# Optimization experiments

Measured on AMD Instinct MI355X. Metric: run time of the kernel, lower is better.

## Reference

```python
import jax, jax.numpy as jnp
import numpy as np

P = 8192          # number of gaussians
H = 256           # image height
W = 256           # image width
TANX = 0.5        # tan(fovx/2)
TANY = 0.5        # tan(fovy/2)
SCALE_MOD = 1.0
CHUNK = 128       # gaussians composited per scan step
FX = W / (2.0 * TANX)   # focal_x, as in forward()
FY = H / (2.0 * TANY)   # focal_y


def setup_inputs() -> dict:
    key = jax.random.key(0)
    k = jax.random.split(key, 6)
    # place gaussians in the camera frustum (camera at origin, looking +z)
    z = jax.random.uniform(k[0], (P,), minval=2.0, maxval=6.0)
    xy = jax.random.normal(k[1], (P, 2)) * 0.4 * (z * TANX)[:, None]
    means3D = jnp.concatenate([xy, z[:, None]], axis=1)
    scales = 0.01 + 0.04 * jax.random.uniform(k[2], (P, 3))
    rotations = jax.random.normal(k[3], (P, 4))  # normalized inside reference
    opacities = 0.05 + 0.9 * jax.random.uniform(k[4], (P, 1))
    colors_precomp = jax.random.uniform(k[5], (P, 3))
    background = jnp.zeros((3,), jnp.float32)
    viewmatrix = jnp.eye(4, dtype=jnp.float32)  # row-vector convention: p' = [p,1] @ V
    znear, zfar = 0.01, 100.0
    Pm = np.zeros((4, 4), np.float32)
    Pm[0, 0] = 1.0 / TANX
    Pm[1, 1] = 1.0 / TANY
    Pm[2, 2] = zfar / (zfar - znear)
    Pm[2, 3] = -(zfar * znear) / (zfar - znear)
    Pm[3, 2] = 1.0
    projmatrix = jnp.asarray(Pm.T)  # row-vector convention (full proj = proj @ view, view = I)
    return dict(means3D=means3D, colors_precomp=colors_precomp, opacities=opacities,
                scales=scales, rotations=rotations, background=background,
                viewmatrix=viewmatrix, projmatrix=projmatrix)


def _quat_to_rot(q):
    q = q / jnp.linalg.norm(q, axis=-1, keepdims=True)
    r, x, y, z = q[:, 0], q[:, 1], q[:, 2], q[:, 3]
    R = jnp.stack([
        1 - 2 * (y * y + z * z), 2 * (x * y - r * z), 2 * (x * z + r * y),
        2 * (x * y + r * z), 1 - 2 * (x * x + z * z), 2 * (y * z - r * x),
        2 * (x * z - r * y), 2 * (y * z + r * x), 1 - 2 * (x * x + y * y)], axis=-1)
    return R.reshape(-1, 3, 3)


def _forward(means3D, colors_precomp, opacities, scales, rotations, background,
             viewmatrix, projmatrix):
    Pn = means3D.shape[0]
    # --- preprocess: 3D covariance from scale/rotation ---
    R = _quat_to_rot(rotations)
    s2 = (scales * SCALE_MOD) ** 2
    Sigma = jnp.einsum('pij,pj,pkj->pik', R, s2, R)  # R diag(s^2) R^T, [P,3,3]
    hom = jnp.concatenate([means3D, jnp.ones((Pn, 1), means3D.dtype)], axis=1)
    p_view = (hom @ viewmatrix)[:, :3]
    p_hom = hom @ projmatrix
    p_proj = p_hom[:, :3] / (p_hom[:, 3:4] + 1e-7)
    # NDC -> pixel centers
    mean2d = jnp.stack([((p_proj[:, 0] + 1.0) * W - 1.0) * 0.5,
                        ((p_proj[:, 1] + 1.0) * H - 1.0) * 0.5], axis=1)
    depths = p_view[:, 2]
    # --- EWA splatting: project covariance to 2D ---
    Rv = viewmatrix[:3, :3]
    cov_cam = jnp.einsum('ji,pjk,kl->pil', Rv, Sigma, Rv)  # Rv^T Sigma Rv
    tz = p_view[:, 2]
    tx = jnp.clip(p_view[:, 0] / tz, -1.3 * TANX, 1.3 * TANX) * tz
    ty = jnp.clip(p_view[:, 1] / tz, -1.3 * TANY, 1.3 * TANY) * tz
    zero = jnp.zeros_like(tz)
    J = jnp.stack([jnp.stack([FX / tz, zero, -FX * tx / tz ** 2], -1),
                   jnp.stack([zero, FY / tz, -FY * ty / tz ** 2], -1)], axis=1)  # [P,2,3]
    cov2d = jnp.einsum('pij,pjk,plk->pil', J, cov_cam, J)
    a = cov2d[:, 0, 0] + 0.3  # low-pass dilation as in 3DGS
    b = cov2d[:, 0, 1]
    c = cov2d[:, 1, 1] + 0.3
    det = a * c - b * b
    conic = jnp.stack([c, -b, a], axis=-1) / det[:, None]
    # --- global depth sort ---
    order = jnp.argsort(depths)
    m2d = mean2d[order]
    con = conic[order]
    col = colors_precomp[order]
    op = opacities[order]
    # --- per-pixel front-to-back alpha compositing ---
    px, py = jnp.meshgrid(jnp.arange(W, dtype=jnp.float32),
                          jnp.arange(H, dtype=jnp.float32))
    pixf = jnp.stack([px.ravel(), py.ravel()], axis=-1)  # [HW,2]
    n_chunks = Pn // CHUNK
    xs = (m2d.reshape(n_chunks, CHUNK, 2), con.reshape(n_chunks, CHUNK, 3),
          col.reshape(n_chunks, CHUNK, 3), op.reshape(n_chunks, CHUNK, 1))

    def step(carry, x):
        accum, T = carry
        m, cn, cl, o = x
        d = m[:, None, :] - pixf[None]  # [C,HW,2]
        power = (-0.5 * (cn[:, 0:1] * d[..., 0] ** 2 + cn[:, 2:3] * d[..., 1] ** 2)
                 - cn[:, 1:2] * d[..., 0] * d[..., 1])
        alpha = jnp.minimum(0.99, o * jnp.exp(power))
        alpha = jnp.where((power > 0.0) | (alpha < 1.0 / 255.0), 0.0, alpha)
        cp = jnp.cumprod(1.0 - alpha, axis=0)  # within-chunk transmittance
        excl = jnp.concatenate([jnp.ones((1, alpha.shape[1]), alpha.dtype), cp[:-1]], 0)
        wgt = alpha * excl * T[None]
        accum = accum + jnp.einsum('cp,cd->pd', wgt, cl)
        return (accum, T * cp[-1]), None

    accum0 = jnp.zeros((H * W, 3), jnp.float32)
    T0 = jnp.ones((H * W,), jnp.float32)
    (accum, T), _ = jax.lax.scan(step, (accum0, T0), xs)
    out = accum + T[:, None] * background[None]
    return out.reshape(H, W, 3).transpose(2, 0, 1)  # [3,H,W]


def reference(means3D, colors_precomp, opacities, scales, rotations, background,
              viewmatrix, projmatrix):
    return _forward(means3D, colors_precomp, opacities, scales, rotations,
                    background, viewmatrix, projmatrix)
```

## Files before the change

### kernel.cpp

```cpp
#include <hip/hip_runtime.h>


#define PN 8192
#define IH 256
#define IW 256


__global__ __launch_bounds__(256) void preprocess_kernel(
    const float* __restrict__ means, const float* __restrict__ colors,
    const float* __restrict__ ops, const float* __restrict__ scales,
    const float* __restrict__ rots, const float* __restrict__ V,
    const float* __restrict__ Pm, float* __restrict__ ws)
{
    int i = blockIdx.x * 256 + threadIdx.x;
    if (i >= PN) return;

    float mx3 = means[3 * i], my3 = means[3 * i + 1], mz3 = means[3 * i + 2];
    float qr = rots[4 * i], qx = rots[4 * i + 1], qy = rots[4 * i + 2], qz = rots[4 * i + 3];
    float qn = 1.0f / sqrtf(qr * qr + qx * qx + qy * qy + qz * qz);
    float r = qr * qn, x = qx * qn, y = qy * qn, z = qz * qn;

    float R00 = 1.f - 2.f * (y * y + z * z), R01 = 2.f * (x * y - r * z), R02 = 2.f * (x * z + r * y);
    float R10 = 2.f * (x * y + r * z), R11 = 1.f - 2.f * (x * x + z * z), R12 = 2.f * (y * z - r * x);
    float R20 = 2.f * (x * z - r * y), R21 = 2.f * (y * z + r * x), R22 = 1.f - 2.f * (x * x + y * y);

    float s0 = scales[3 * i];     s0 *= s0;
    float s1 = scales[3 * i + 1]; s1 *= s1;
    float s2 = scales[3 * i + 2]; s2 *= s2;

    float Sg[3][3];
    Sg[0][0] = R00 * R00 * s0 + R01 * R01 * s1 + R02 * R02 * s2;
    Sg[0][1] = R00 * R10 * s0 + R01 * R11 * s1 + R02 * R12 * s2;
    Sg[0][2] = R00 * R20 * s0 + R01 * R21 * s1 + R02 * R22 * s2;
    Sg[1][1] = R10 * R10 * s0 + R11 * R11 * s1 + R12 * R12 * s2;
    Sg[1][2] = R10 * R20 * s0 + R11 * R21 * s1 + R12 * R22 * s2;
    Sg[2][2] = R20 * R20 * s0 + R21 * R21 * s1 + R22 * R22 * s2;
    Sg[1][0] = Sg[0][1]; Sg[2][0] = Sg[0][2]; Sg[2][1] = Sg[1][2];

    float pv0 = mx3 * V[0] + my3 * V[4] + mz3 * V[8]  + V[12];
    float pv1 = mx3 * V[1] + my3 * V[5] + mz3 * V[9]  + V[13];
    float pv2 = mx3 * V[2] + my3 * V[6] + mz3 * V[10] + V[14];
    float ph0 = mx3 * Pm[0] + my3 * Pm[4] + mz3 * Pm[8]  + Pm[12];
    float ph1 = mx3 * Pm[1] + my3 * Pm[5] + mz3 * Pm[9]  + Pm[13];
    float ph3 = mx3 * Pm[3] + my3 * Pm[7] + mz3 * Pm[11] + Pm[15];
    float pw = 1.0f / (ph3 + 1e-7f);
    float m2x = ((ph0 * pw + 1.0f) * (float)IW - 1.0f) * 0.5f;
    float m2y = ((ph1 * pw + 1.0f) * (float)IH - 1.0f) * 0.5f;

    float Rv[3][3];
#pragma unroll
    for (int rr = 0; rr < 3; ++rr)
#pragma unroll
        for (int cc2 = 0; cc2 < 3; ++cc2) Rv[rr][cc2] = V[rr * 4 + cc2];
    float M[3][3];
#pragma unroll
    for (int j = 0; j < 3; ++j)
#pragma unroll
        for (int l = 0; l < 3; ++l)
            M[j][l] = Sg[j][0] * Rv[0][l] + Sg[j][1] * Rv[1][l] + Sg[j][2] * Rv[2][l];
    float cc[3][3];
#pragma unroll
    for (int ii = 0; ii < 3; ++ii)
#pragma unroll
        for (int l = 0; l < 3; ++l)
            cc[ii][l] = Rv[0][ii] * M[0][l] + Rv[1][ii] * M[1][l] + Rv[2][ii] * M[2][l];

    const float FX = 256.0f, FY = 256.0f;
    float tz = pv2;
    float itz = 1.0f / tz;
    float limx = 0.65f, limy = 0.65f;
    float txz = fminf(fmaxf(pv0 * itz, -limx), limx);
    float tyz = fminf(fmaxf(pv1 * itz, -limy), limy);
    float tx = txz * tz, ty = tyz * tz;
    float J00 = FX * itz, J02 = -FX * tx * itz * itz;
    float J11 = FY * itz, J12 = -FY * ty * itz * itz;

    float u00 = J00 * cc[0][0] + J02 * cc[2][0];
    float u01 = J00 * cc[0][1] + J02 * cc[2][1];
    float u02 = J00 * cc[0][2] + J02 * cc[2][2];
    float u11 = J11 * cc[1][1] + J12 * cc[2][1];
    float u12 = J11 * cc[1][2] + J12 * cc[2][2];
    float cov00 = u00 * J00 + u02 * J02;
    float cov01 = u01 * J11 + u02 * J12;
    float cov11 = u11 * J11 + u12 * J12;

    float a = cov00 + 0.3f;
    float b = cov01;
    float c = cov11 + 0.3f;
    float det = a * c - b * b;
    float idet = 1.0f / det;
    float cA = c * idet;
    float cB = -b * idet;
    float cC = a * idet;

    float ex = sqrtf(11.2f * a);
    float ey = sqrtf(11.2f * c);
    int x0 = max(0,  (int)floorf((m2x - ex) * 0.125f));
    int x1 = min(31, (int)floorf((m2x + ex) * 0.125f));
    int y0 = max(0,  (int)floorf((m2y - ey) * 0.125f));
    int y1 = min(31, (int)floorf((m2y + ey) * 0.125f));
    x0 = min(x0, 31); y0 = min(y0, 31); x1 = max(x1, 0); y1 = max(y1, 0);
    unsigned box = (unsigned)x0 | ((unsigned)x1 << 8) | ((unsigned)y0 << 16) | ((unsigned)y1 << 24);

    ws[i] = pv2;
    float4* preA = (float4*)(ws + PN);
    float4* preB = (float4*)(ws + 5 * PN);
    preA[i] = make_float4(m2x, m2y, cA, cB);
    preB[i] = make_float4(cC, ops[i], colors[3 * i], colors[3 * i + 1]);
    ws[9 * PN + i] = colors[3 * i + 2];
    ((unsigned*)(ws + 10 * PN))[i] = box;
}

__global__ __launch_bounds__(256) void sort_scatter_kernel(float* __restrict__ ws)
{
    const float* dep = ws;
    const float4* d4 = (const float4*)ws;
    int lane = threadIdx.x & 63;
    int wid = threadIdx.x >> 6;
    int gbase = blockIdx.x * 16 + wid * 4;

    float di0 = dep[gbase], di1 = dep[gbase + 1], di2 = dep[gbase + 2], di3 = dep[gbase + 3];
    int r0 = 0, r1 = 0, r2 = 0, r3 = 0;
#pragma unroll 4
    for (int k = 0; k < 32; ++k) {
        int j4 = k * 64 + lane;
        float4 d = d4[j4];
        int jb = j4 * 4;
        r0 += (d.x < di0) || (d.x == di0 && (jb    ) < gbase);
        r0 += (d.y < di0) || (d.y == di0 && (jb + 1) < gbase);
        r0 += (d.z < di0) || (d.z == di0 && (jb + 2) < gbase);
        r0 += (d.w < di0) || (d.w == di0 && (jb + 3) < gbase);
        r1 += (d.x < di1) || (d.x == di1 && (jb    ) < gbase + 1);
        r1 += (d.y < di1) || (d.y == di1 && (jb + 1) < gbase + 1);
        r1 += (d.z < di1) || (d.z == di1 && (jb + 2) < gbase + 1);
        r1 += (d.w < di1) || (d.w == di1 && (jb + 3) < gbase + 1);
        r2 += (d.x < di2) || (d.x == di2 && (jb    ) < gbase + 2);
        r2 += (d.y < di2) || (d.y == di2 && (jb + 1) < gbase + 2);
        r2 += (d.z < di2) || (d.z == di2 && (jb + 2) < gbase + 2);
        r2 += (d.w < di2) || (d.w == di2 && (jb + 3) < gbase + 2);
        r3 += (d.x < di3) || (d.x == di3 && (jb    ) < gbase + 3);
        r3 += (d.y < di3) || (d.y == di3 && (jb + 1) < gbase + 3);
        r3 += (d.z < di3) || (d.z == di3 && (jb + 2) < gbase + 3);
        r3 += (d.w < di3) || (d.w == di3 && (jb + 3) < gbase + 3);
    }
#pragma unroll
    for (int off = 1; off < 64; off <<= 1) {
        r0 += __shfl_xor(r0, off);
        r1 += __shfl_xor(r1, off);
        r2 += __shfl_xor(r2, off);
        r3 += __shfl_xor(r3, off);
    }
    if (lane < 4) {
        int rk = (lane == 0) ? r0 : (lane == 1) ? r1 : (lane == 2) ? r2 : r3;
        int i = gbase + lane;
        const float4* preA = (const float4*)(ws + PN);
        const float4* preB = (const float4*)(ws + 5 * PN);
        float4* sA = (float4*)(ws + 11 * PN);
        float4* sB = (float4*)(ws + 15 * PN);
        sA[rk] = preA[i];
        sB[rk] = preB[i];
        ws[19 * PN + rk] = ws[9 * PN + i];
        ((unsigned*)(ws + 20 * PN))[rk] = ((const unsigned*)(ws + 10 * PN))[i];
    }
}

__global__ __launch_bounds__(256) void raster_kernel(
    const float* __restrict__ ws, const float* __restrict__ bg,
    float* __restrict__ out)
{
    __shared__ float4 lsA[4][256];
    __shared__ float4 lsB[4][256];
    __shared__ float  lsb[4][256];
    volatile __shared__ float waveT[4];

    int tid = threadIdx.x;
    int lane = tid & 63, w = tid >> 6;
    int bq = blockIdx.x >> 8;
    int tileIdx = (bq << 8) | ((blockIdx.x & 255) ^ ((bq * 9) & 31));
    int tileX = tileIdx & 31, tileY = tileIdx >> 5;
    int px = tileX * 8 + (lane & 7), py = tileY * 8 + (lane >> 3);
    float pxf = (float)px, pyf = (float)py;

    const float4* sA = (const float4*)(ws + 11 * PN);
    const float4* sB = (const float4*)(ws + 15 * PN);
    const float* sb = ws + 19 * PN;
    const unsigned* sbox = (const unsigned*)(ws + 20 * PN);

    if (tid < 4) waveT[tid] = 1.0f;
    __syncthreads();

    float T = 1.0f, ar = 0.0f, ag = 0.0f, ab = 0.0f;

    for (int chunk = w * 8; chunk < w * 8 + 8; ++chunk) {
        float pre = 1.0f;
        for (int q = 0; q < w; ++q) pre *= waveT[q];
        if (pre < 1e-4f) break;

        int base = chunk * 256;
        unsigned long long wv[4];
#pragma unroll
        for (int k = 0; k < 4; ++k) {
            unsigned bx = sbox[base + k * 64 + lane];
            bool ov = (tileX >= (int)(bx & 255)) & (tileX <= (int)((bx >> 8) & 255)) &
                      (tileY >= (int)((bx >> 16) & 255)) & (tileY <= (int)(bx >> 24));
            wv[k] = __ballot(ov);
        }
        if (!(wv[0] | wv[1] | wv[2] | wv[3])) continue;

        int cnt = 0;
#pragma unroll
        for (int k = 0; k < 4; ++k) {
            unsigned long long wk = wv[k];
            if ((wk >> lane) & 1ull) {
                int slot = cnt + (int)__popcll(wk & ((1ull << lane) - 1ull));
                int g = base + k * 64 + lane;
                lsA[w][slot] = sA[g];
                lsB[w][slot] = sB[g];
                lsb[w][slot] = sb[g];
            }
            cnt += (int)__popcll(wk);
        }
        asm volatile("s_waitcnt lgkmcnt(0)" ::: "memory");

        int j = 0;
        for (; j + 1 < cnt; j += 2) {
            float4 A0 = lsA[w][j],     B0 = lsB[w][j];
            float4 A1 = lsA[w][j + 1], B1 = lsB[w][j + 1];
            float b0 = lsb[w][j], b1 = lsb[w][j + 1];
            float dx0 = A0.x - pxf, dy0 = A0.y - pyf;
            float dx1 = A1.x - pxf, dy1 = A1.y - pyf;
            float p0 = -0.5f * (A0.z * dx0 * dx0 + B0.x * dy0 * dy0) - A0.w * dx0 * dy0;
            float p1 = -0.5f * (A1.z * dx1 * dx1 + B1.x * dy1 * dy1) - A1.w * dx1 * dy1;
            float al0 = fminf(0.99f, B0.y * __expf(p0));
            float al1 = fminf(0.99f, B1.y * __expf(p1));
            float a0 = ((p0 > 0.0f) | (al0 < (1.0f / 255.0f))) ? 0.0f : al0;
            float a1 = ((p1 > 0.0f) | (al1 < (1.0f / 255.0f))) ? 0.0f : al1;
            float w0 = a0 * T;
            float Tm = T * (1.0f - a0);
            float w1 = a1 * Tm;
            ar = fmaf(w0, B0.z, ar); ar = fmaf(w1, B1.z, ar);
            ag = fmaf(w0, B0.w, ag); ag = fmaf(w1, B1.w, ag);
            ab = fmaf(w0, b0, ab);   ab = fmaf(w1, b1, ab);
            T = Tm * (1.0f - a1);
        }
        if (j < cnt) {
            float4 A = lsA[w][j];
            float4 B = lsB[w][j];
            float bcol = lsb[w][j];
            float dx = A.x - pxf, dy = A.y - pyf;
            float power = -0.5f * (A.z * dx * dx + B.x * dy * dy) - A.w * dx * dy;
            float alpha = fminf(0.99f, B.y * __expf(power));
            float a2 = ((power > 0.0f) | (alpha < (1.0f / 255.0f))) ? 0.0f : alpha;
            float wgt = a2 * T;
            ar = fmaf(wgt, B.z, ar);
            ag = fmaf(wgt, B.w, ag);
            ab = fmaf(wgt, bcol, ab);
            T *= (1.0f - a2);
        }
        asm volatile("s_waitcnt lgkmcnt(0)" ::: "memory");

        if (__all(T < 1e-5f)) break;

        float tmax = T;
#pragma unroll
        for (int off = 1; off < 64; off <<= 1) tmax = fmaxf(tmax, __shfl_xor(tmax, off));
        if (lane == 0) waveT[w] = tmax;
    }

    lsb[w][lane * 4 + 0] = ar;
    lsb[w][lane * 4 + 1] = ag;
    lsb[w][lane * 4 + 2] = ab;
    lsb[w][lane * 4 + 3] = T;
    __syncthreads();

    if (w == 0) {
        float A0 = 0.f, A1 = 0.f, A2 = 0.f, Tt = 1.f;
#pragma unroll
        for (int q = 0; q < 4; ++q) {
            A0 += Tt * lsb[q][lane * 4 + 0];
            A1 += Tt * lsb[q][lane * 4 + 1];
            A2 += Tt * lsb[q][lane * 4 + 2];
            Tt *= lsb[q][lane * 4 + 3];
        }
        int pidx = py * IW + px;
        out[pidx]               = A0 + Tt * bg[0];
        out[IH * IW + pidx]     = A1 + Tt * bg[1];
        out[2 * IH * IW + pidx] = A2 + Tt * bg[2];
    }
}

extern "C" void kernel_launch(void* const* d_in, const int* in_sizes, int n_in,
                              void* d_out, int out_size, void* d_ws, size_t ws_size,
                              hipStream_t stream) {
    const float* means  = (const float*)d_in[0];
    const float* colors = (const float*)d_in[1];
    const float* ops    = (const float*)d_in[2];
    const float* scales = (const float*)d_in[3];
    const float* rots   = (const float*)d_in[4];
    const float* bg     = (const float*)d_in[5];
    const float* viewm  = (const float*)d_in[6];
    const float* projm  = (const float*)d_in[7];
    float* out = (float*)d_out;
    float* ws  = (float*)d_ws;

    hipLaunchKernelGGL(preprocess_kernel, dim3(PN / 256), dim3(256), 0, stream,
                       means, colors, ops, scales, rots, viewm, projm, ws);
    hipLaunchKernelGGL(sort_scatter_kernel, dim3(PN / 16), dim3(256), 0, stream, ws);
    hipLaunchKernelGGL(raster_kernel, dim3(1024), dim3(256), 0, stream, ws, bg, out);
}
```

Baseline: 107.6 us.

## Pack two tiles per 512-thread block and unroll compositing by four

The raster kernel now runs 512-thread blocks that each cover two 8x8 tiles (left and right halves of a tile row), with four waves per tile, and launches half as many blocks. The swizzled tile ordering is replaced by a plain row-major mapping. The inner compositing loop is unrolled to four gaussians per iteration, with the transmittance products precomputed so the weights depend less on a serial chain. This raises LDS use per block, drops the L2-locality swizzle, and gives slightly different float rounding in the transmittance product.

```diff
diff --git a/kernel.cpp b/kernel.cpp
--- a/kernel.cpp
+++ b/kernel.cpp
@@ -164,20 +164,21 @@
     }
 }
 
-__global__ __launch_bounds__(256) void raster_kernel(
+__global__ __launch_bounds__(512, 4) void raster_kernel(
     const float* __restrict__ ws, const float* __restrict__ bg,
     float* __restrict__ out)
 {
-    __shared__ float4 lsA[4][256];
-    __shared__ float4 lsB[4][256];
-    __shared__ float  lsb[4][256];
-    volatile __shared__ float waveT[4];
+    __shared__ float4 lsA[8][256];
+    __shared__ float4 lsB[8][256];
+    __shared__ float  lsb[8][256];
+    volatile __shared__ float waveT[8];
 
     int tid = threadIdx.x;
     int lane = tid & 63, w = tid >> 6;
-    int bq = blockIdx.x >> 8;
-    int tileIdx = (bq << 8) | ((blockIdx.x & 255) ^ ((bq * 9) & 31));
-    int tileX = tileIdx & 31, tileY = tileIdx >> 5;
+    int g = w >> 2, wl = w & 3;
+    int yt = blockIdx.x >> 4;
+    int xh = blockIdx.x & 15;
+    int tileX = xh + g * 16, tileY = yt;
     int px = tileX * 8 + (lane & 7), py = tileY * 8 + (lane >> 3);
     float pxf = (float)px, pyf = (float)py;
 
@@ -186,14 +187,14 @@
     const float* sb = ws + 19 * PN;
     const unsigned* sbox = (const unsigned*)(ws + 20 * PN);
 
-    if (tid < 4) waveT[tid] = 1.0f;
+    if (tid < 8) waveT[tid] = 1.0f;
     __syncthreads();
 
     float T = 1.0f, ar = 0.0f, ag = 0.0f, ab = 0.0f;
 
-    for (int chunk = w * 8; chunk < w * 8 + 8; ++chunk) {
+    for (int chunk = wl * 8; chunk < wl * 8 + 8; ++chunk) {
         float pre = 1.0f;
-        for (int q = 0; q < w; ++q) pre *= waveT[q];
+        for (int q = g * 4; q < w; ++q) pre *= waveT[q];
         if (pre < 1e-4f) break;
 
         int base = chunk * 256;
@@ -213,37 +214,53 @@
             unsigned long long wk = wv[k];
             if ((wk >> lane) & 1ull) {
                 int slot = cnt + (int)__popcll(wk & ((1ull << lane) - 1ull));
-                int g = base + k * 64 + lane;
-                lsA[w][slot] = sA[g];
-                lsB[w][slot] = sB[g];
-                lsb[w][slot] = sb[g];
+                int gg = base + k * 64 + lane;
+                lsA[w][slot] = sA[gg];
+                lsB[w][slot] = sB[gg];
+                lsb[w][slot] = sb[gg];
             }
             cnt += (int)__popcll(wk);
         }
         asm volatile("s_waitcnt lgkmcnt(0)" ::: "memory");
 
         int j = 0;
-        for (; j + 1 < cnt; j += 2) {
+        for (; j + 3 < cnt; j += 4) {
             float4 A0 = lsA[w][j],     B0 = lsB[w][j];
             float4 A1 = lsA[w][j + 1], B1 = lsB[w][j + 1];
-            float b0 = lsb[w][j], b1 = lsb[w][j + 1];
+            float4 A2 = lsA[w][j + 2], B2 = lsB[w][j + 2];
+            float4 A3 = lsA[w][j + 3], B3 = lsB[w][j + 3];
+            float c0 = lsb[w][j], c1 = lsb[w][j + 1], c2 = lsb[w][j + 2], c3 = lsb[w][j + 3];
             float dx0 = A0.x - pxf, dy0 = A0.y - pyf;
             float dx1 = A1.x - pxf, dy1 = A1.y - pyf;
+            float dx2 = A2.x - pxf, dy2 = A2.y - pyf;
+            float dx3 = A3.x - pxf, dy3 = A3.y - pyf;
             float p0 = -0.5f * (A0.z * dx0 * dx0 + B0.x * dy0 * dy0) - A0.w * dx0 * dy0;
             float p1 = -0.5f * (A1.z * dx1 * dx1 + B1.x * dy1 * dy1) - A1.w * dx1 * dy1;
-            float al0 = fminf(0.99f, B0.y * __expf(p0));
-            float al1 = fminf(0.99f, B1.y * __expf(p1));
-            float a0 = ((p0 > 0.0f) | (al0 < (1.0f / 255.0f))) ? 0.0f : al0;
-            float a1 = ((p1 > 0.0f) | (al1 < (1.0f / 255.0f))) ? 0.0f : al1;
+            float p2 = -0.5f * (A2.z * dx2 * dx2 + B2.x * dy2 * dy2) - A2.w * dx2 * dy2;
+            float p3 = -0.5f * (A3.z * dx3 * dx3 + B3.x * dy3 * dy3) - A3.w * dx3 * dy3;
+            float e0 = fminf(0.99f, B0.y * __expf(p0));
+            float e1 = fminf(0.99f, B1.y * __expf(p1));
+            float e2 = fminf(0.99f, B2.y * __expf(p2));
+            float e3 = fminf(0.99f, B3.y * __expf(p3));
+            float a0 = ((p0 > 0.0f) | (e0 < (1.0f / 255.0f))) ? 0.0f : e0;
+            float a1 = ((p1 > 0.0f) | (e1 < (1.0f / 255.0f))) ? 0.0f : e1;
+            float a2 = ((p2 > 0.0f) | (e2 < (1.0f / 255.0f))) ? 0.0f : e2;
+            float a3 = ((p3 > 0.0f) | (e3 < (1.0f / 255.0f))) ? 0.0f : e3;
+            float t0 = 1.0f - a0, t1 = 1.0f - a1, t2 = 1.0f - a2, t3 = 1.0f - a3;
+            float c01 = t0 * t1, c012 = c01 * t2;
             float w0 = a0 * T;
-            float Tm = T * (1.0f - a0);
-            float w1 = a1 * Tm;
+            float w1 = a1 * (T * t0);
+            float w2 = a2 * (T * c01);
+            float w3 = a3 * (T * c012);
             ar = fmaf(w0, B0.z, ar); ar = fmaf(w1, B1.z, ar);
+            ar = fmaf(w2, B2.z, ar); ar = fmaf(w3, B3.z, ar);
             ag = fmaf(w0, B0.w, ag); ag = fmaf(w1, B1.w, ag);
-            ab = fmaf(w0, b0, ab);   ab = fmaf(w1, b1, ab);
-            T = Tm * (1.0f - a1);
-        }
-        if (j < cnt) {
+            ag = fmaf(w2, B2.w, ag); ag = fmaf(w3, B3.w, ag);
+            ab = fmaf(w0, c0, ab);   ab = fmaf(w1, c1, ab);
+            ab = fmaf(w2, c2, ab);   ab = fmaf(w3, c3, ab);
+            T *= (c012 * t3);
+        }
+        for (; j < cnt; ++j) {
             float4 A = lsA[w][j];
             float4 B = lsB[w][j];
             float bcol = lsb[w][j];
@@ -273,14 +290,14 @@
     lsb[w][lane * 4 + 3] = T;
     __syncthreads();
 
-    if (w == 0) {
+    if (wl == 0) {
         float A0 = 0.f, A1 = 0.f, A2 = 0.f, Tt = 1.f;
 #pragma unroll
         for (int q = 0; q < 4; ++q) {
-            A0 += Tt * lsb[q][lane * 4 + 0];
-            A1 += Tt * lsb[q][lane * 4 + 1];
-            A2 += Tt * lsb[q][lane * 4 + 2];
-            Tt *= lsb[q][lane * 4 + 3];
+            A0 += Tt * lsb[g * 4 + q][lane * 4 + 0];
+            A1 += Tt * lsb[g * 4 + q][lane * 4 + 1];
+            A2 += Tt * lsb[g * 4 + q][lane * 4 + 2];
+            Tt *= lsb[g * 4 + q][lane * 4 + 3];
         }
         int pidx = py * IW + px;
         out[pidx]               = A0 + Tt * bg[0];
@@ -306,5 +323,5 @@
     hipLaunchKernelGGL(preprocess_kernel, dim3(PN / 256), dim3(256), 0, stream,
                        means, colors, ops, scales, rots, viewm, projm, ws);
     hipLaunchKernelGGL(sort_scatter_kernel, dim3(PN / 16), dim3(256), 0, stream, ws);
-    hipLaunchKernelGGL(raster_kernel, dim3(1024), dim3(256), 0, stream, ws, bg, out);
+    hipLaunchKernelGGL(raster_kernel, dim3(512), dim3(512), 0, stream, ws, bg, out);
 }
```

Measured after the change: 106.4 us, median of 2. Within noise of the previous version (-1.1%).
